# Kernel tuning notes

Measured on AMD Instinct MI355X. Metric: run time of the kernel, lower is better.

## Reference

```python
import jax, jax.numpy as jnp
import numpy as np

BS, NWP, D, NEXP, H, OUT = 32768, 10, 256, 6, 64, 2

def setup_inputs() -> dict:
    key = jax.random.key(0)
    ks = jax.random.split(key, 8)
    x = jax.random.normal(ks[0], (BS, NWP, D), dtype=jnp.float32)
    measurements = jax.random.randint(ks[1], (BS, 1), 0, NEXP, dtype=jnp.int32)
    rank_embed = 0.02 * jax.random.normal(ks[2], (1, NWP, D), dtype=jnp.float32)
    # Linear weights stored as [in, out] for einsum; biases [out]
    W1 = 0.05 * jax.random.normal(ks[3], (NEXP, D, H), dtype=jnp.float32)
    b1 = 0.05 * jax.random.normal(ks[4], (NEXP, H), dtype=jnp.float32)
    W2 = 0.05 * jax.random.normal(ks[5], (NEXP, H, OUT), dtype=jnp.float32)
    b2 = 0.05 * jax.random.normal(ks[6], (NEXP, OUT), dtype=jnp.float32)
    return {"x": x, "measurements": measurements, "rank_embed": rank_embed,
            "W1": W1, "b1": b1, "W2": W2, "b2": b2}

def reference(x, measurements, rank_embed, W1, b1, W2, b2):
    command = measurements[:, 0]                      # [bs] int in [0,6)
    xr = x + rank_embed                               # [bs, 10, d]
    # Dense 6-way expert MLP (matches original: all heads computed for all samples)
    h = jax.nn.relu(jnp.einsum('bnd,edh->benh', xr, W1) + b1[None, :, None, :])  # [bs,6,10,64]
    wp = jnp.einsum('benh,eho->beno', h, W2) + b2[None, :, None, :]              # [bs,6,10,2]
    sel = jnp.take_along_axis(wp, command[:, None, None, None].astype(jnp.int32), axis=1)[:, 0]  # [bs,10,2]
    return jnp.cumsum(sel, axis=1)
```

## Files before the change

### kernel.cpp

```cpp
#include <hip/hip_runtime.h>
#include <hip/hip_bf16.h>

#define BS 32768
#define NWP 10
#define DD 256
#define NEXP 6
#define HH 64
#define OUT_DIM 2
#define MB 64

typedef short bf16x8 __attribute__((ext_vector_type(8)));
typedef float f32x4 __attribute__((ext_vector_type(4)));

__device__ inline short bfs(float f) {
  __hip_bfloat16 h = __float2bfloat16(f);
  return __builtin_bit_cast(short, h);
}

__global__ __launch_bounds__(1024) void bucket_k(const int* __restrict__ cmd,
                                                 int* __restrict__ counts,
                                                 unsigned short* __restrict__ lists) {
  __shared__ int wcnt[16][NEXP];
  __shared__ int wbase[16][NEXP];
  const int tid = threadIdx.x;
  const int w = tid >> 6, lane = tid & 63;
  const int b = blockIdx.x * 1024 + tid;
  const int e = cmd[b];
  #pragma unroll
  for (int ee = 0; ee < NEXP; ++ee) {
    unsigned long long m = __ballot(e == ee);
    if (lane == 0) wcnt[w][ee] = __popcll(m);
  }
  __syncthreads();
  if (tid < NEXP) {
    int tot = 0, pf[16];
    #pragma unroll
    for (int ww = 0; ww < 16; ++ww) { pf[ww] = tot; tot += wcnt[ww][tid]; }
    const int bb = atomicAdd(&counts[tid], tot);
    #pragma unroll
    for (int ww = 0; ww < 16; ++ww) wbase[ww][tid] = bb + pf[ww];
  }
  __syncthreads();
  #pragma unroll
  for (int ee = 0; ee < NEXP; ++ee) {
    unsigned long long m = __ballot(e == ee);
    if (e == ee) {
      const int nbelow = __popcll(m & ((1ull << lane) - 1ull));
      lists[ee * BS + wbase[w][ee] + nbelow] = (unsigned short)b;
    }
  }
}

__global__ void prep_k(const float* __restrict__ W1,
                       const float* __restrict__ re,
                       const float* __restrict__ b1,
                       short* __restrict__ W1T,
                       float* __restrict__ rw) {
  const int e = blockIdx.x;
  const int part = blockIdx.y;
  if (part < 8) {
    const int h = part * 8 + (threadIdx.x >> 5);
    const int d0 = (threadIdx.x & 31) * 8;
    const float* wp = W1 + (size_t)e * DD * HH + h;
    bf16x8 v;
    #pragma unroll
    for (int i = 0; i < 8; ++i) v[i] = bfs(wp[(size_t)(d0 + i) * HH]);
    *(bf16x8*)(W1T + ((size_t)e * HH + h) * DD + d0) = v;
  } else {
    for (int i = threadIdx.x; i < NWP * HH; i += 256) {
      const int n = i >> 6, h = i & 63;
      const float* rp = re + (size_t)n * DD;
      const float* wp = W1 + (size_t)e * DD * HH + h;
      float s = b1[e * HH + h];
      for (int d = 0; d < DD; ++d) s += rp[d] * wp[(size_t)d * HH];
      rw[((size_t)e * NWP + n) * HH + h] = s;
    }
  }
}

__global__ __launch_bounds__(256, 2) void moe_gemm_k(
    const float* __restrict__ x,
    const short* __restrict__ W1T,
    const float* __restrict__ rwg,
    const float* __restrict__ W2,
    const float* __restrict__ b2,
    const int* __restrict__ counts,
    const unsigned short* __restrict__ lists,
    float* __restrict__ out)
{
  __shared__ short Xa[4][16 * DD];
  __shared__ float rwl[NWP][68];
  __shared__ float w2l[HH * OUT_DIM];
  __shared__ float po[MB * NWP][2];

  const int e = blockIdx.y;
  const int cnt = counts[e];
  const int start = blockIdx.x * MB;
  if (start >= cnt) return;
  const int nb = min(MB, cnt - start);
  const int nrows = nb * NWP;

  const int tid = threadIdx.x;
  const int lane = tid & 63;
  const int wv = tid >> 6;
  const int arow = lane & 15;
  const int ag = lane >> 4;

  bf16x8 Wf[4][8];
  {
    const short* wb = W1T + ((size_t)e * HH + arow) * DD + ag * 8;
    #pragma unroll
    for (int nt = 0; nt < 4; ++nt)
      #pragma unroll
      for (int ks = 0; ks < 8; ++ks)
        Wf[nt][ks] = *(const bf16x8*)(wb + (size_t)(nt * 16) * DD + ks * 32);
  }
  for (int i = tid; i < NWP * HH; i += 256)
    rwl[i >> 6][i & 63] = rwg[(size_t)e * NWP * HH + i];
  if (tid < HH * OUT_DIM) w2l[tid] = W2[(size_t)e * HH * OUT_DIM + tid];

  int bid_reg = (int)lists[e * BS + start + lane];

  __syncthreads();

  short* Xw = &Xa[wv][0];
  const int ntile = (nrows + 15) >> 4;

  for (int t = wv; t < ntile; t += 4) {
    #pragma unroll
    for (int r = 0; r < 16; ++r) {
      const int rowc = min(t * 16 + r, nrows - 1);
      const int item = rowc / NWP;
      const int nn = rowc - item * NWP;
      const int gb = __shfl(bid_reg, item);
      const float4 xv = *(const float4*)(x + ((size_t)gb * NWP + nn) * DD + lane * 4);
      short4 pk = make_short4(bfs(xv.x), bfs(xv.y), bfs(xv.z), bfs(xv.w));
      *(short4*)&Xw[r * DD + ((lane * 4) ^ ((r & 7) << 3))] = pk;
    }

    f32x4 acc[4] = {{0,0,0,0},{0,0,0,0},{0,0,0,0},{0,0,0,0}};
    #pragma unroll
    for (int ks = 0; ks < 8; ++ks) {
      const int kidx = ks * 32 + ag * 8;
      const bf16x8 bx = *(const bf16x8*)&Xw[arow * DD + (kidx ^ ((arow & 7) << 3))];
      #pragma unroll
      for (int nt = 0; nt < 4; ++nt)
        acc[nt] = __builtin_amdgcn_mfma_f32_16x16x32_bf16(Wf[nt][ks], bx, acc[nt], 0, 0, 0);
    }

    const int row = t * 16 + arow;
    const int rowc = min(row, nrows - 1);
    const int nn = rowc - (rowc / NWP) * NWP;
    float p0 = 0.f, p1 = 0.f;
    #pragma unroll
    for (int nt = 0; nt < 4; ++nt) {
      const int h0 = nt * 16 + ag * 4;
      const float4 rv = *(const float4*)&rwl[nn][h0];
      const float4 wa = *(const float4*)&w2l[h0 * 2];
      const float4 wb = *(const float4*)&w2l[h0 * 2 + 4];
      const float h0v = fmaxf(acc[nt][0] + rv.x, 0.f);
      const float h1v = fmaxf(acc[nt][1] + rv.y, 0.f);
      const float h2v = fmaxf(acc[nt][2] + rv.z, 0.f);
      const float h3v = fmaxf(acc[nt][3] + rv.w, 0.f);
      p0 += h0v * wa.x + h1v * wa.z + h2v * wb.x + h3v * wb.z;
      p1 += h0v * wa.y + h1v * wa.w + h2v * wb.y + h3v * wb.w;
    }
    p0 += __shfl_xor(p0, 16); p1 += __shfl_xor(p1, 16);
    p0 += __shfl_xor(p0, 32); p1 += __shfl_xor(p1, 32);
    if (ag == 0 && row < nrows) {
      po[row][0] = p0;
      po[row][1] = p1;
    }
  }

  __syncthreads();

  if (tid < nb) {
    const int gb = (int)lists[e * BS + start + tid];
    const float bb0 = b2[e * OUT_DIM + 0];
    const float bb1 = b2[e * OUT_DIM + 1];
    float v[NWP * OUT_DIM];
    float s0 = 0.f, s1 = 0.f;
    #pragma unroll
    for (int n = 0; n < NWP; ++n) {
      s0 += po[tid * NWP + n][0] + bb0;
      s1 += po[tid * NWP + n][1] + bb1;
      v[n * 2 + 0] = s0;
      v[n * 2 + 1] = s1;
    }
    float4* op = (float4*)(out + (size_t)gb * NWP * OUT_DIM);
    #pragma unroll
    for (int q = 0; q < 5; ++q)
      op[q] = make_float4(v[q * 4], v[q * 4 + 1], v[q * 4 + 2], v[q * 4 + 3]);
  }
}

extern "C" void kernel_launch(void* const* d_in, const int* in_sizes, int n_in,
                              void* d_out, int out_size, void* d_ws, size_t ws_size,
                              hipStream_t stream) {
  const float* x          = (const float*)d_in[0];
  const int*   meas       = (const int*)d_in[1];
  const float* rank_embed = (const float*)d_in[2];
  const float* W1         = (const float*)d_in[3];
  const float* b1         = (const float*)d_in[4];
  const float* W2         = (const float*)d_in[5];
  const float* b2         = (const float*)d_in[6];
  float* out = (float*)d_out;

  int* counts = (int*)d_ws;
  unsigned short* lists = (unsigned short*)((char*)d_ws + 4096);
  short* W1T = (short*)((char*)d_ws + (448 << 10));
  float* rw  = (float*)((char*)d_ws + (704 << 10));

  hipMemsetAsync(d_ws, 0, 256, stream);
  bucket_k<<<BS / 1024, 1024, 0, stream>>>(meas, counts, lists);
  prep_k<<<dim3(NEXP, 9), 256, 0, stream>>>(W1, rank_embed, b1, W1T, rw);
  dim3 gg((BS + MB - 1) / MB, NEXP);
  moe_gemm_k<<<gg, 256, 0, stream>>>(x, W1T, rw, W2, b2, counts, lists, out);
}
```

Baseline: 114.0 us.

## Replace per-expert grid with persistent blocks pulling tiles from an atomic work queue

Adds a small kernel that turns the per-expert token counts into a flat list of (expert, start) work items. The GEMM kernel now runs as 512 persistent blocks that claim items through an atomic counter, instead of a 2D grid in which most blocks exit immediately. The tile size is halved to 32 tokens so there are more items to balance across blocks. The cost is one extra launch, an atomic and a block barrier per item, and reloading the W1 fragments and per-expert constants for every item rather than once per block.

```diff
diff --git a/kernel.cpp b/kernel.cpp
--- a/kernel.cpp
+++ b/kernel.cpp
@@ -7,7 +7,7 @@
 #define NEXP 6
 #define HH 64
 #define OUT_DIM 2
-#define MB 64
+#define MB 32
 
 typedef short bf16x8 __attribute__((ext_vector_type(8)));
 typedef float f32x4 __attribute__((ext_vector_type(4)));
@@ -78,13 +78,34 @@
   }
 }
 
+__global__ void build_q_k(const int* __restrict__ counts, int* __restrict__ qmeta) {
+  __shared__ int base[NEXP + 1];
+  if (threadIdx.x == 0) {
+    int tot = 0;
+    #pragma unroll
+    for (int e = 0; e < NEXP; ++e) {
+      base[e] = tot;
+      tot += (counts[e] + MB - 1) / MB;
+    }
+    base[NEXP] = tot;
+    qmeta[17] = tot;
+  }
+  __syncthreads();
+  #pragma unroll
+  for (int e = 0; e < NEXP; ++e) {
+    const int ne = base[e + 1] - base[e];
+    for (int j = threadIdx.x; j < ne; j += blockDim.x)
+      qmeta[32 + base[e] + j] = (e << 16) | (j * MB);
+  }
+}
+
 __global__ __launch_bounds__(256, 2) void moe_gemm_k(
     const float* __restrict__ x,
     const short* __restrict__ W1T,
     const float* __restrict__ rwg,
     const float* __restrict__ W2,
     const float* __restrict__ b2,
-    const int* __restrict__ counts,
+    int* __restrict__ qmeta,
     const unsigned short* __restrict__ lists,
     float* __restrict__ out)
 {
@@ -92,106 +113,114 @@
   __shared__ float rwl[NWP][68];
   __shared__ float w2l[HH * OUT_DIM];
   __shared__ float po[MB * NWP][2];
-
-  const int e = blockIdx.y;
-  const int cnt = counts[e];
-  const int start = blockIdx.x * MB;
-  if (start >= cnt) return;
-  const int nb = min(MB, cnt - start);
-  const int nrows = nb * NWP;
+  __shared__ int s_wi;
 
   const int tid = threadIdx.x;
   const int lane = tid & 63;
   const int wv = tid >> 6;
   const int arow = lane & 15;
   const int ag = lane >> 4;
-
-  bf16x8 Wf[4][8];
-  {
-    const short* wb = W1T + ((size_t)e * HH + arow) * DD + ag * 8;
-    #pragma unroll
-    for (int nt = 0; nt < 4; ++nt)
-      #pragma unroll
-      for (int ks = 0; ks < 8; ++ks)
-        Wf[nt][ks] = *(const bf16x8*)(wb + (size_t)(nt * 16) * DD + ks * 32);
-  }
-  for (int i = tid; i < NWP * HH; i += 256)
-    rwl[i >> 6][i & 63] = rwg[(size_t)e * NWP * HH + i];
-  if (tid < HH * OUT_DIM) w2l[tid] = W2[(size_t)e * HH * OUT_DIM + tid];
-
-  int bid_reg = (int)lists[e * BS + start + lane];
-
-  __syncthreads();
-
-  short* Xw = &Xa[wv][0];
-  const int ntile = (nrows + 15) >> 4;
-
-  for (int t = wv; t < ntile; t += 4) {
-    #pragma unroll
-    for (int r = 0; r < 16; ++r) {
-      const int rowc = min(t * 16 + r, nrows - 1);
-      const int item = rowc / NWP;
-      const int nn = rowc - item * NWP;
-      const int gb = __shfl(bid_reg, item);
-      const float4 xv = *(const float4*)(x + ((size_t)gb * NWP + nn) * DD + lane * 4);
-      short4 pk = make_short4(bfs(xv.x), bfs(xv.y), bfs(xv.z), bfs(xv.w));
-      *(short4*)&Xw[r * DD + ((lane * 4) ^ ((r & 7) << 3))] = pk;
-    }
-
-    f32x4 acc[4] = {{0,0,0,0},{0,0,0,0},{0,0,0,0},{0,0,0,0}};
-    #pragma unroll
-    for (int ks = 0; ks < 8; ++ks) {
-      const int kidx = ks * 32 + ag * 8;
-      const bf16x8 bx = *(const bf16x8*)&Xw[arow * DD + (kidx ^ ((arow & 7) << 3))];
+  const int qtot = qmeta[17];
+
+  for (;;) {
+    if (tid == 0) s_wi = atomicAdd(&qmeta[16], 1);
+    __syncthreads();
+    const int wi = s_wi;
+    if (wi >= qtot) break;
+    const int ent = qmeta[32 + wi];
+    const int e = ent >> 16;
+    const int start = ent & 0xffff;
+    const int cnt = qmeta[e];
+    const int nb = min(MB, cnt - start);
+    const int nrows = nb * NWP;
+
+    bf16x8 Wf[4][8];
+    {
+      const short* wb = W1T + ((size_t)e * HH + arow) * DD + ag * 8;
       #pragma unroll
       for (int nt = 0; nt < 4; ++nt)
-        acc[nt] = __builtin_amdgcn_mfma_f32_16x16x32_bf16(Wf[nt][ks], bx, acc[nt], 0, 0, 0);
-    }
-
-    const int row = t * 16 + arow;
-    const int rowc = min(row, nrows - 1);
-    const int nn = rowc - (rowc / NWP) * NWP;
-    float p0 = 0.f, p1 = 0.f;
-    #pragma unroll
-    for (int nt = 0; nt < 4; ++nt) {
-      const int h0 = nt * 16 + ag * 4;
-      const float4 rv = *(const float4*)&rwl[nn][h0];
-      const float4 wa = *(const float4*)&w2l[h0 * 2];
-      const float4 wb = *(const float4*)&w2l[h0 * 2 + 4];
-      const float h0v = fmaxf(acc[nt][0] + rv.x, 0.f);
-      const float h1v = fmaxf(acc[nt][1] + rv.y, 0.f);
-      const float h2v = fmaxf(acc[nt][2] + rv.z, 0.f);
-      const float h3v = fmaxf(acc[nt][3] + rv.w, 0.f);
-      p0 += h0v * wa.x + h1v * wa.z + h2v * wb.x + h3v * wb.z;
-      p1 += h0v * wa.y + h1v * wa.w + h2v * wb.y + h3v * wb.w;
-    }
-    p0 += __shfl_xor(p0, 16); p1 += __shfl_xor(p1, 16);
-    p0 += __shfl_xor(p0, 32); p1 += __shfl_xor(p1, 32);
-    if (ag == 0 && row < nrows) {
-      po[row][0] = p0;
-      po[row][1] = p1;
-    }
-  }
-
-  __syncthreads();
-
-  if (tid < nb) {
-    const int gb = (int)lists[e * BS + start + tid];
-    const float bb0 = b2[e * OUT_DIM + 0];
-    const float bb1 = b2[e * OUT_DIM + 1];
-    float v[NWP * OUT_DIM];
-    float s0 = 0.f, s1 = 0.f;
-    #pragma unroll
-    for (int n = 0; n < NWP; ++n) {
-      s0 += po[tid * NWP + n][0] + bb0;
-      s1 += po[tid * NWP + n][1] + bb1;
-      v[n * 2 + 0] = s0;
-      v[n * 2 + 1] = s1;
-    }
-    float4* op = (float4*)(out + (size_t)gb * NWP * OUT_DIM);
-    #pragma unroll
-    for (int q = 0; q < 5; ++q)
-      op[q] = make_float4(v[q * 4], v[q * 4 + 1], v[q * 4 + 2], v[q * 4 + 3]);
+        #pragma unroll
+        for (int ks = 0; ks < 8; ++ks)
+          Wf[nt][ks] = *(const bf16x8*)(wb + (size_t)(nt * 16) * DD + ks * 32);
+    }
+    for (int i = tid; i < NWP * HH; i += 256)
+      rwl[i >> 6][i & 63] = rwg[(size_t)e * NWP * HH + i];
+    if (tid < HH * OUT_DIM) w2l[tid] = W2[(size_t)e * HH * OUT_DIM + tid];
+
+    int bid_reg = (int)lists[e * BS + start + lane];
+
+    __syncthreads();
+
+    short* Xw = &Xa[wv][0];
+    const int ntile = (nrows + 15) >> 4;
+
+    for (int t = wv; t < ntile; t += 4) {
+      #pragma unroll
+      for (int r = 0; r < 16; ++r) {
+        const int rowc = min(t * 16 + r, nrows - 1);
+        const int item = rowc / NWP;
+        const int nn = rowc - item * NWP;
+        const int gb = __shfl(bid_reg, item);
+        const float4 xv = *(const float4*)(x + ((size_t)gb * NWP + nn) * DD + lane * 4);
+        short4 pk = make_short4(bfs(xv.x), bfs(xv.y), bfs(xv.z), bfs(xv.w));
+        *(short4*)&Xw[r * DD + ((lane * 4) ^ ((r & 7) << 3))] = pk;
+      }
+
+      f32x4 acc[4] = {{0,0,0,0},{0,0,0,0},{0,0,0,0},{0,0,0,0}};
+      #pragma unroll
+      for (int ks = 0; ks < 8; ++ks) {
+        const int kidx = ks * 32 + ag * 8;
+        const bf16x8 bx = *(const bf16x8*)&Xw[arow * DD + (kidx ^ ((arow & 7) << 3))];
+        #pragma unroll
+        for (int nt = 0; nt < 4; ++nt)
+          acc[nt] = __builtin_amdgcn_mfma_f32_16x16x32_bf16(Wf[nt][ks], bx, acc[nt], 0, 0, 0);
+      }
+
+      const int row = t * 16 + arow;
+      const int rowc = min(row, nrows - 1);
+      const int nn = rowc - (rowc / NWP) * NWP;
+      float p0 = 0.f, p1 = 0.f;
+      #pragma unroll
+      for (int nt = 0; nt < 4; ++nt) {
+        const int h0 = nt * 16 + ag * 4;
+        const float4 rv = *(const float4*)&rwl[nn][h0];
+        const float4 wa = *(const float4*)&w2l[h0 * 2];
+        const float4 wb = *(const float4*)&w2l[h0 * 2 + 4];
+        const float h0v = fmaxf(acc[nt][0] + rv.x, 0.f);
+        const float h1v = fmaxf(acc[nt][1] + rv.y, 0.f);
+        const float h2v = fmaxf(acc[nt][2] + rv.z, 0.f);
+        const float h3v = fmaxf(acc[nt][3] + rv.w, 0.f);
+        p0 += h0v * wa.x + h1v * wa.z + h2v * wb.x + h3v * wb.z;
+        p1 += h0v * wa.y + h1v * wa.w + h2v * wb.y + h3v * wb.w;
+      }
+      p0 += __shfl_xor(p0, 16); p1 += __shfl_xor(p1, 16);
+      p0 += __shfl_xor(p0, 32); p1 += __shfl_xor(p1, 32);
+      if (ag == 0 && row < nrows) {
+        po[row][0] = p0;
+        po[row][1] = p1;
+      }
+    }
+
+    __syncthreads();
+
+    if (tid < nb) {
+      const int gb = (int)lists[e * BS + start + tid];
+      const float bb0 = b2[e * OUT_DIM + 0];
+      const float bb1 = b2[e * OUT_DIM + 1];
+      float v[NWP * OUT_DIM];
+      float s0 = 0.f, s1 = 0.f;
+      #pragma unroll
+      for (int n = 0; n < NWP; ++n) {
+        s0 += po[tid * NWP + n][0] + bb0;
+        s1 += po[tid * NWP + n][1] + bb1;
+        v[n * 2 + 0] = s0;
+        v[n * 2 + 1] = s1;
+      }
+      float4* op = (float4*)(out + (size_t)gb * NWP * OUT_DIM);
+      #pragma unroll
+      for (int q = 0; q < 5; ++q)
+        op[q] = make_float4(v[q * 4], v[q * 4 + 1], v[q * 4 + 2], v[q * 4 + 3]);
+    }
   }
 }
 
@@ -207,14 +236,14 @@
   const float* b2         = (const float*)d_in[6];
   float* out = (float*)d_out;
 
-  int* counts = (int*)d_ws;
-  unsigned short* lists = (unsigned short*)((char*)d_ws + 4096);
-  short* W1T = (short*)((char*)d_ws + (448 << 10));
-  float* rw  = (float*)((char*)d_ws + (704 << 10));
-
-  hipMemsetAsync(d_ws, 0, 256, stream);
-  bucket_k<<<BS / 1024, 1024, 0, stream>>>(meas, counts, lists);
+  int* qmeta = (int*)d_ws;
+  unsigned short* lists = (unsigned short*)((char*)d_ws + 8192);
+  short* W1T = (short*)((char*)d_ws + (452 << 10));
+  float* rw  = (float*)((char*)d_ws + (708 << 10));
+
+  hipMemsetAsync(d_ws, 0, 8192, stream);
+  bucket_k<<<BS / 1024, 1024, 0, stream>>>(meas, qmeta, lists);
   prep_k<<<dim3(NEXP, 9), 256, 0, stream>>>(W1, rank_embed, b1, W1T, rw);
-  dim3 gg((BS + MB - 1) / MB, NEXP);
-  moe_gemm_k<<<gg, 256, 0, stream>>>(x, W1T, rw, W2, b2, counts, lists, out);
-}
+  build_q_k<<<1, 256, 0, stream>>>(qmeta, qmeta);
+  moe_gemm_k<<<512, 256, 0, stream>>>(x, W1T, rw, W2, b2, qmeta, lists, out);
+}
```

Result: slower. 193.7 us (+69.9%).
